# Performance work log

Measured on AMD Instinct MI355X. Metric: run time of the kernel, lower is better.

Reference implementation:

```python
import jax, jax.numpy as jnp
import numpy as np
from jax import lax

# Dimensions (match init_kwargs / input_specs)
S, I, NO = 64, 128, 64      # num_states, num_inputs, num_outputs
K, D = 64, 64               # stack_size, stack_dim
B, T_LEN = 64, 256          # batch of sequences, sequence length
PSTR_THRESH = 0.01          # push/pop gating threshold from original code


def setup_inputs() -> dict:
    key = jax.random.key(0)
    k0, k1, k2, k3, k4, k5 = jax.random.split(key, 6)
    return {
        "input_seq": jax.random.randint(k0, (B, T_LEN), 0, I),
        "T": jax.random.normal(k1, (S, I, D, S), jnp.float32) * 0.1,
        "O": jax.random.normal(k2, (S, I, D, NO), jnp.float32) * 0.1,
        "push_gate": jax.random.normal(k3, (S, I, 1), jnp.float32) * 0.1,
        "pop_gate": jax.random.normal(k4, (S, I, 1), jnp.float32) * 0.1,
        "push_value": jax.random.normal(k5, (S, I, D), jnp.float32) * 0.1,
        "init_logits": jnp.zeros((S,), jnp.float32),
    }


def _run_seq(seq, T, O, push_gate, pop_gate, push_value, init_logits):
    """Process one sequence of int symbols; returns [T_LEN, NO] output probs."""
    state0 = jax.nn.softmax(init_logits)                    # (S,)
    content0 = jnp.zeros((K, D), T.dtype)                   # stack buffer
    pointer0 = jnp.zeros((K,), T.dtype).at[0].set(1.0)      # soft stack pointer

    def step(carry, inp):
        state, content, pointer = carry
        stack_top = pointer @ content                       # (D,) soft read

        # Output: mixture over states of softmax(stack_top @ O[s, inp])
        out_logits = jnp.einsum('d,sdo->so', stack_top, O[:, inp])
        out_prob = state @ jax.nn.softmax(out_logits, axis=-1)  # (NO,)

        # Push/pop strengths: scalars; original uses .item() so they are detached
        push_s = lax.stop_gradient(jax.nn.sigmoid(push_gate[:, inp, 0] @ state))
        pop_s = lax.stop_gradient(jax.nn.sigmoid(pop_gate[:, inp, 0] @ state))
        push_v = jnp.tanh(state @ push_value[:, inp, :])    # (D,) keeps grad

        # Pop (only applied if pop_s > threshold, as in original)
        shifted_down = jnp.concatenate([pointer[1:], jnp.zeros((1,), pointer.dtype)])
        ptr_pop = pop_s * shifted_down + (1.0 - pop_s) * pointer
        pointer = jnp.where(pop_s > PSTR_THRESH, ptr_pop, pointer)

        # Push (only applied if push_s > threshold)
        shifted_up = jnp.concatenate([jnp.zeros((1,), pointer.dtype), pointer[:-1]])
        ptr_push = push_s * shifted_up + (1.0 - push_s) * pointer
        w = ptr_push[:, None]                                # (K,1) write weights
        do_push = push_s > PSTR_THRESH
        pointer = jnp.where(do_push, ptr_push, pointer)
        content = jnp.where(do_push, content * (1.0 - w) + push_v[None, :] * w, content)

        # State transition uses PRE-update stack_top (as in original)
        trans_logits = jnp.einsum('d,sdn->sn', stack_top, T[:, inp])
        new_state = state @ jax.nn.softmax(trans_logits, axis=-1)
        return (new_state, content, pointer), out_prob

    _, outs = lax.scan(step, (state0, content0, pointer0), seq)
    return outs


def reference(input_seq, T, O, push_gate, pop_gate, push_value, init_logits):
    run = lambda seq: _run_seq(seq, T, O, push_gate, pop_gate, push_value, init_logits)
    return jax.vmap(run)(input_seq)  # (B, T_LEN, NO)
```

## Files before the change

kernel.cpp:

```cpp
#include <hip/hip_runtime.h>
#include <math.h>

namespace {
constexpr int cS = 64, cI = 128, cNO = 64, cK = 64, cD = 64, cB = 64, cT = 256;
constexpr float cTH = 0.01f;
constexpr int NTASK = cB * cT;
constexpr int NSPLIT = 8;
typedef float vf4 __attribute__((ext_vector_type(4)));

__device__ inline void st_agent(float* p, float v) {
    __hip_atomic_store(p, v, __ATOMIC_RELAXED, __HIP_MEMORY_SCOPE_AGENT);
}
__device__ inline float ld_agent(const float* p) {
    return __hip_atomic_load(p, __ATOMIC_RELAXED, __HIP_MEMORY_SCOPE_AGENT);
}

__global__ __launch_bounds__(256, 2)
void p1_kernel(const int* __restrict__ seq,
               const float* __restrict__ Tm,
               const float* __restrict__ pgate,
               const float* __restrict__ qgate,
               const float* __restrict__ pval,
               const float* __restrict__ initl,
               float* __restrict__ stbuf,
               int* __restrict__ cnt,
               float* __restrict__ gpart)
{
    const int b  = blockIdx.x >> 3;
    const int jw = blockIdx.x & 7;
    const int tid = threadIdx.x;
    const int wave = tid >> 6, lane = tid & 63;
    const int dq = lane >> 4, o4 = lane & 15;

    __shared__ float s_state[cS], s_stack[cD], s_pushv[cD], s_pvpart[cD];
    __shared__ float s_ptr[cK], s_w[cK];
    __shared__ float s_content[cK][cD];
    __shared__ float s_redA[4][64], s_redB[4][64], s_npart[4][64];
    __shared__ int   s_seq[cT];
    __shared__ float s_push, s_pop;

    if (wave == 0) {
        float v = initl[lane];
        float m = v;
        #pragma unroll
        for (int sh = 1; sh < 64; sh <<= 1) m = fmaxf(m, __shfl_xor(m, sh));
        float e = expf(v - m);
        float s = e;
        #pragma unroll
        for (int sh = 1; sh < 64; sh <<= 1) s += __shfl_xor(s, sh);
        s_state[lane] = e / s;
    } else if (wave == 1) {
        s_ptr[lane] = (lane == 0) ? 1.0f : 0.0f;
    }
    for (int i = tid; i < cK * cD; i += 256) (&s_content[0][0])[i] = 0.f;
    s_seq[tid] = seq[b * cT + tid];
    __syncthreads();

    for (int t = 0; t < cT; ++t) {
        const int inp = s_seq[t];

        {
            float accA = 0.f;
            #pragma unroll
            for (int j = 0; j < 16; ++j) {
                int k = wave * 16 + j;
                accA += s_ptr[k] * s_content[k][lane];
            }
            float accB = 0.f;
            #pragma unroll
            for (int j = 0; j < 2; ++j) {
                int k = jw * 8 + wave * 2 + j;
                accB += s_state[k] * pval[((size_t)k * cI + inp) * cD + lane];
            }
            s_redA[wave][lane] = accA;
            s_redB[wave][lane] = accB;
        }
        __syncthreads();

        float* sb = stbuf + (size_t)(b * cT + t) * 128;
        if (wave == 0) {
            float a = s_redA[0][lane] + s_redA[1][lane] + s_redA[2][lane] + s_redA[3][lane];
            s_stack[lane] = a;
            if (jw == 0) { sb[lane] = a; sb[64 + lane] = s_state[lane]; }
        } else if (wave == 1) {
            s_pvpart[lane] = s_redB[0][lane] + s_redB[1][lane] + s_redB[2][lane] + s_redB[3][lane];
        } else if (wave == 2) {
            float v = pgate[lane * cI + inp] * s_state[lane];
            #pragma unroll
            for (int sh = 1; sh < 64; sh <<= 1) v += __shfl_xor(v, sh);
            if (lane == 0) s_push = 1.0f / (1.0f + expf(-v));
        } else {
            float v = qgate[lane * cI + inp] * s_state[lane];
            #pragma unroll
            for (int sh = 1; sh < 64; sh <<= 1) v += __shfl_xor(v, sh);
            if (lane == 0) s_pop = 1.0f / (1.0f + expf(-v));
        }
        __syncthreads();

        {
            float xs[16];
            #pragma unroll
            for (int i = 0; i < 16; ++i) xs[i] = s_stack[dq * 16 + i];

            const int sA = jw * 8 + wave * 2;
            const int sB = sA + 1;
            const vf4* rpA = reinterpret_cast<const vf4*>(
                Tm + (size_t)(sA * cI + inp) * (cD * cS)) + o4;
            const vf4* rpB = reinterpret_cast<const vf4*>(
                Tm + (size_t)(sB * cI + inp) * (cD * cS)) + o4;
            vf4 va[16], vb[16];
            #pragma unroll
            for (int i = 0; i < 16; ++i) {
                va[i] = rpA[(dq * 16 + i) * 16];
                vb[i] = rpB[(dq * 16 + i) * 16];
            }
            vf4 aA, aB;
            aA.x = 0.f; aA.y = 0.f; aA.z = 0.f; aA.w = 0.f;
            aB.x = 0.f; aB.y = 0.f; aB.z = 0.f; aB.w = 0.f;
            #pragma unroll
            for (int i = 0; i < 16; ++i) {
                float x = xs[i];
                aA.x = fmaf(x, va[i].x, aA.x); aA.y = fmaf(x, va[i].y, aA.y);
                aA.z = fmaf(x, va[i].z, aA.z); aA.w = fmaf(x, va[i].w, aA.w);
                aB.x = fmaf(x, vb[i].x, aB.x); aB.y = fmaf(x, vb[i].y, aB.y);
                aB.z = fmaf(x, vb[i].z, aB.z); aB.w = fmaf(x, vb[i].w, aB.w);
            }
            #pragma unroll
            for (int m = 16; m < 64; m <<= 1) {
                aA.x += __shfl_xor(aA.x, m); aA.y += __shfl_xor(aA.y, m);
                aA.z += __shfl_xor(aA.z, m); aA.w += __shfl_xor(aA.w, m);
                aB.x += __shfl_xor(aB.x, m); aB.y += __shfl_xor(aB.y, m);
                aB.z += __shfl_xor(aB.z, m); aB.w += __shfl_xor(aB.w, m);
            }
            float mA = fmaxf(fmaxf(aA.x, aA.y), fmaxf(aA.z, aA.w));
            float mB = fmaxf(fmaxf(aB.x, aB.y), fmaxf(aB.z, aB.w));
            #pragma unroll
            for (int m = 1; m < 16; m <<= 1) {
                mA = fmaxf(mA, __shfl_xor(mA, m));
                mB = fmaxf(mB, __shfl_xor(mB, m));
            }
            vf4 eA, eB;
            eA.x = expf(aA.x - mA); eA.y = expf(aA.y - mA);
            eA.z = expf(aA.z - mA); eA.w = expf(aA.w - mA);
            eB.x = expf(aB.x - mB); eB.y = expf(aB.y - mB);
            eB.z = expf(aB.z - mB); eB.w = expf(aB.w - mB);
            float smA = eA.x + eA.y + eA.z + eA.w;
            float smB = eB.x + eB.y + eB.z + eB.w;
            #pragma unroll
            for (int m = 1; m < 16; m <<= 1) {
                smA += __shfl_xor(smA, m);
                smB += __shfl_xor(smB, m);
            }
            float cA = s_state[sA] / smA;
            float cB = s_state[sB] / smB;
            vf4 nacc;
            nacc.x = cA * eA.x + cB * eB.x;
            nacc.y = cA * eA.y + cB * eB.y;
            nacc.z = cA * eA.z + cB * eB.z;
            nacc.w = cA * eA.w + cB * eB.w;
            if (dq == 0) {
                s_npart[wave][o4 * 4 + 0] = nacc.x;
                s_npart[wave][o4 * 4 + 1] = nacc.y;
                s_npart[wave][o4 * 4 + 2] = nacc.z;
                s_npart[wave][o4 * 4 + 3] = nacc.w;
            }
        }
        __syncthreads();

        if (wave == 0) {
            float* gq = gpart + ((size_t)(b * 2 + (t & 1)) * NSPLIT + jw) * 128;
            float np = s_npart[0][lane] + s_npart[1][lane] + s_npart[2][lane] + s_npart[3][lane];
            st_agent(gq + lane, np);
            st_agent(gq + 64 + lane, s_pvpart[lane]);
            asm volatile("s_waitcnt vmcnt(0)" ::: "memory");
            int* c = cnt + b * cT + t;
            if (lane == 0)
                __hip_atomic_fetch_add(c, 1, __ATOMIC_RELAXED, __HIP_MEMORY_SCOPE_AGENT);
            while (__hip_atomic_load(c, __ATOMIC_RELAXED, __HIP_MEMORY_SCOPE_AGENT) < NSPLIT) {}
            const float* gb = gpart + (size_t)(b * 2 + (t & 1)) * NSPLIT * 128;
            float ns = 0.f, pvs = 0.f;
            #pragma unroll
            for (int q = 0; q < NSPLIT; ++q) {
                ns  += ld_agent(gb + q * 128 + lane);
                pvs += ld_agent(gb + q * 128 + 64 + lane);
            }
            s_state[lane] = ns;
            s_pushv[lane] = tanhf(pvs);
        } else if (wave == 1) {
            float p  = s_ptr[lane];
            float sd = (lane < cK - 1) ? s_ptr[lane + 1] : 0.f;
            float pop = s_pop;
            float ppo = pop * sd + (1.f - pop) * p;
            float p2  = (pop > cTH) ? ppo : p;
            float su  = __shfl_up(p2, 1);
            if (lane == 0) su = 0.f;
            float push = s_push;
            float ppu = push * su + (1.f - push) * p2;
            s_w[lane] = ppu;
            s_ptr[lane] = (push > cTH) ? ppu : p2;
        }
        __syncthreads();

        if (s_push > cTH) {
            #pragma unroll
            for (int it = 0; it < 16; ++it) {
                int idx = tid + it * 256;
                int k = idx >> 6, d = idx & 63;
                float w = s_w[k];
                s_content[k][d] = s_content[k][d] * (1.f - w) + s_pushv[d] * w;
            }
        }
        __syncthreads();
    }
}

__global__ void k_count(const int* __restrict__ seq, int* __restrict__ counts) {
    int i = blockIdx.x * 256 + threadIdx.x;
    if (i < NTASK) atomicAdd(&counts[seq[i]], 1);
}
__global__ void k_scan(const int* __restrict__ counts, int* __restrict__ offsets,
                       int* __restrict__ cursor) {
    const int lane = threadIdx.x & 63;
    int c0 = counts[lane], c1 = counts[64 + lane];
    int s0 = c0, s1 = c1;
    #pragma unroll
    for (int m = 1; m < 64; m <<= 1) {
        int t0 = __shfl_up(s0, m);
        int t1 = __shfl_up(s1, m);
        if (lane >= m) { s0 += t0; s1 += t1; }
    }
    int tot0 = __shfl(s0, 63);
    int e0 = s0 - c0;
    int e1 = tot0 + s1 - c1;
    offsets[lane] = e0;       cursor[lane] = e0;
    offsets[64 + lane] = e1;  cursor[64 + lane] = e1;
    if (lane == 63) offsets[128] = tot0 + __shfl(s1, 63);
}
__global__ void k_scatter(const int* __restrict__ seq, int* __restrict__ cursor,
                          int* __restrict__ tasks) {
    int i = blockIdx.x * 256 + threadIdx.x;
    if (i < NTASK) {
        int pos = atomicAdd(&cursor[seq[i]], 1);
        tasks[pos] = i;
    }
}

__global__ __launch_bounds__(512, 2)
void p2_kernel(const float* __restrict__ Om,
               const float* __restrict__ stbuf,
               const int* __restrict__ offsets,
               const int* __restrict__ tasks,
               float* __restrict__ out)
{
    const int g = blockIdx.x >> 1, h = blockIdx.x & 1;
    const int tid = threadIdx.x, wave = tid >> 6, lane = tid & 63;
    const int dq = lane >> 4, o4 = lane & 15;

    const int beg = offsets[g], end = offsets[g + 1];
    const int n = end - beg, half = (n + 1) >> 1;
    const int hbeg = beg + h * half;
    const int hend = h ? end : (beg + half);
    const int cnt = hend - hbeg;
    if (cnt <= 0) return;
    const int nsweep = (cnt + 63) >> 6;

    __shared__ vf4 sO[2][1024];

    const vf4* O0 = reinterpret_cast<const vf4*>(Om) + (size_t)g * 1024;
    const size_t rowstride = (size_t)cI * 1024;

    for (int sweep = 0; sweep < nsweep; ++sweep) {
        int   tsk[8];
        bool  val[8];
        float stv[8][16];
        float sstate[8];
        vf4   acc[8];
        #pragma unroll
        for (int u = 0; u < 8; ++u) {
            int idx = hbeg + sweep * 64 + (u >> 2) * 32 + wave * 4 + (u & 3);
            bool v = idx < hend;
            val[u] = v;
            int id = tasks[v ? idx : hbeg];
            id = __builtin_amdgcn_readfirstlane(id);
            tsk[u] = id;
            const float* sp = stbuf + (size_t)id * 128;
            #pragma unroll
            for (int i = 0; i < 16; ++i) stv[u][i] = sp[dq * 16 + i];
            sstate[u] = sp[64 + lane];
            acc[u].x = 0.f; acc[u].y = 0.f; acc[u].z = 0.f; acc[u].w = 0.f;
        }

        vf4 r0 = __builtin_nontemporal_load(O0 + (size_t)tid * 2);
        vf4 r1 = __builtin_nontemporal_load(O0 + (size_t)tid * 2 + 1);

        for (int s = 0; s < cS; ++s) {
            sO[s & 1][tid * 2]     = r0;
            sO[s & 1][tid * 2 + 1] = r1;
            __syncthreads();
            if (s + 1 < cS) {
                const vf4* nr = O0 + (size_t)(s + 1) * rowstride;
                r0 = __builtin_nontemporal_load(nr + (size_t)tid * 2);
                r1 = __builtin_nontemporal_load(nr + (size_t)tid * 2 + 1);
            }
            vf4 part[8];
            #pragma unroll
            for (int u = 0; u < 8; ++u) { part[u].x = 0.f; part[u].y = 0.f; part[u].z = 0.f; part[u].w = 0.f; }
            #pragma unroll
            for (int i = 0; i < 16; ++i) {
                vf4 ovi = sO[s & 1][(dq * 16 + i) * 16 + o4];
                #pragma unroll
                for (int u = 0; u < 8; ++u) {
                    float x = stv[u][i];
                    part[u].x = fmaf(x, ovi.x, part[u].x);
                    part[u].y = fmaf(x, ovi.y, part[u].y);
                    part[u].z = fmaf(x, ovi.z, part[u].z);
                    part[u].w = fmaf(x, ovi.w, part[u].w);
                }
            }
            #pragma unroll
            for (int u = 0; u < 8; ++u) {
                vf4 a = part[u];
                #pragma unroll
                for (int m = 16; m < 64; m <<= 1) {
                    a.x += __shfl_xor(a.x, m); a.y += __shfl_xor(a.y, m);
                    a.z += __shfl_xor(a.z, m); a.w += __shfl_xor(a.w, m);
                }
                float mx = fmaxf(fmaxf(a.x, a.y), fmaxf(a.z, a.w));
                #pragma unroll
                for (int m = 1; m < 16; m <<= 1) mx = fmaxf(mx, __shfl_xor(mx, m));
                vf4 e;
                e.x = expf(a.x - mx); e.y = expf(a.y - mx);
                e.z = expf(a.z - mx); e.w = expf(a.w - mx);
                float sm = e.x + e.y + e.z + e.w;
                #pragma unroll
                for (int m = 1; m < 16; m <<= 1) sm += __shfl_xor(sm, m);
                float coef = __shfl(sstate[u], s) / sm;
                acc[u].x = fmaf(coef, e.x, acc[u].x);
                acc[u].y = fmaf(coef, e.y, acc[u].y);
                acc[u].z = fmaf(coef, e.z, acc[u].z);
                acc[u].w = fmaf(coef, e.w, acc[u].w);
            }
        }
        #pragma unroll
        for (int u = 0; u < 8; ++u) {
            if (val[u] && dq == 0) {
                float* op = out + (size_t)tsk[u] * cNO + o4 * 4;
                op[0] = acc[u].x; op[1] = acc[u].y; op[2] = acc[u].z; op[3] = acc[u].w;
            }
        }
    }
}

__global__ __launch_bounds__(512, 1)
void fpt_mono(const int* __restrict__ seq, const float* __restrict__ Tm,
              const float* __restrict__ Om, const float* __restrict__ pgate,
              const float* __restrict__ qgate, const float* __restrict__ pval,
              const float* __restrict__ initl, float* __restrict__ out)
{
    const int b = blockIdx.x;
    const int tid = threadIdx.x;
    const int wave = tid >> 6, lane = tid & 63;
    const int dq = lane >> 4, o4 = lane & 15;

    __shared__ float s_state[cS], s_nstate[cS], s_stack[cD], s_pushv[cD];
    __shared__ float s_ptr[cK], s_ptr2[cK], s_w[cK];
    __shared__ float s_content[cK][cD];
    __shared__ float s_redA[8][64], s_redB[8][64];
    __shared__ float s_opart[4][cNO], s_npart[4][cS];
    __shared__ float s_push, s_pop;

    if (wave == 0) {
        float v = initl[lane];
        float m = v;
        #pragma unroll
        for (int sh = 1; sh < 64; sh <<= 1) m = fmaxf(m, __shfl_xor(m, sh));
        float e = expf(v - m);
        float s = e;
        #pragma unroll
        for (int sh = 1; sh < 64; sh <<= 1) s += __shfl_xor(s, sh);
        s_state[lane] = e / s;
    } else if (wave == 1) s_ptr[lane] = (lane == 0) ? 1.0f : 0.0f;
    for (int idx = tid; idx < cK * cD; idx += 512) (&s_content[0][0])[idx] = 0.0f;
    __syncthreads();

    for (int t = 0; t < cT; ++t) {
        const int inp = seq[b * cT + t];
        {
            float accA = 0.f, accB = 0.f;
            #pragma unroll
            for (int j = 0; j < 8; ++j) {
                int k = wave * 8 + j;
                accA += s_ptr[k] * s_content[k][lane];
                accB += s_state[k] * pval[(k * cI + inp) * cD + lane];
            }
            s_redA[wave][lane] = accA;
            s_redB[wave][lane] = accB;
        }
        __syncthreads();
        if (wave == 0) {
            float a = 0.f;
            #pragma unroll
            for (int g = 0; g < 8; ++g) a += s_redA[g][lane];
            s_stack[lane] = a;
        } else if (wave == 1) {
            float a = 0.f;
            #pragma unroll
            for (int g = 0; g < 8; ++g) a += s_redB[g][lane];
            s_pushv[lane] = tanhf(a);
        } else if (wave == 2) {
            float v = pgate[lane * cI + inp] * s_state[lane];
            #pragma unroll
            for (int sh = 1; sh < 64; sh <<= 1) v += __shfl_xor(v, sh);
            if (lane == 0) s_push = 1.0f / (1.0f + expf(-v));
        } else if (wave == 3) {
            float v = qgate[lane * cI + inp] * s_state[lane];
            #pragma unroll
            for (int sh = 1; sh < 64; sh <<= 1) v += __shfl_xor(v, sh);
            if (lane == 0) s_pop = 1.0f / (1.0f + expf(-v));
        }
        __syncthreads();
        {
            const bool isO = (wave < 4);
            const int w4 = wave & 3;
            const float* Mbase = isO ? Om : Tm;
            float xs[16];
            #pragma unroll
            for (int i = 0; i < 16; ++i) xs[i] = s_stack[dq * 16 + i];
            float4 oacc = make_float4(0.f, 0.f, 0.f, 0.f);
            for (int r = 0; r < 16; ++r) {
                const int s = w4 * 16 + r;
                const float4* rowp =
                    reinterpret_cast<const float4*>(Mbase + (size_t)(s * cI + inp) * (cD * 64)) + o4;
                float4 acc = make_float4(0.f, 0.f, 0.f, 0.f);
                #pragma unroll
                for (int i = 0; i < 16; ++i) {
                    float4 mv = rowp[(dq * 16 + i) * 16];
                    float xd = xs[i];
                    acc.x = fmaf(xd, mv.x, acc.x); acc.y = fmaf(xd, mv.y, acc.y);
                    acc.z = fmaf(xd, mv.z, acc.z); acc.w = fmaf(xd, mv.w, acc.w);
                }
                #pragma unroll
                for (int m = 16; m < 64; m <<= 1) {
                    acc.x += __shfl_xor(acc.x, m); acc.y += __shfl_xor(acc.y, m);
                    acc.z += __shfl_xor(acc.z, m); acc.w += __shfl_xor(acc.w, m);
                }
                float mx = fmaxf(fmaxf(acc.x, acc.y), fmaxf(acc.z, acc.w));
                #pragma unroll
                for (int m = 1; m < 16; m <<= 1) mx = fmaxf(mx, __shfl_xor(mx, m));
                float4 e;
                e.x = expf(acc.x - mx); e.y = expf(acc.y - mx);
                e.z = expf(acc.z - mx); e.w = expf(acc.w - mx);
                float sm = e.x + e.y + e.z + e.w;
                #pragma unroll
                for (int m = 1; m < 16; m <<= 1) sm += __shfl_xor(sm, m);
                float coef = s_state[s] / sm;
                oacc.x = fmaf(coef, e.x, oacc.x); oacc.y = fmaf(coef, e.y, oacc.y);
                oacc.z = fmaf(coef, e.z, oacc.z); oacc.w = fmaf(coef, e.w, oacc.w);
            }
            if (dq == 0) {
                float* dst = isO ? &s_opart[w4][0] : &s_npart[w4][0];
                dst[o4 * 4 + 0] = oacc.x; dst[o4 * 4 + 1] = oacc.y;
                dst[o4 * 4 + 2] = oacc.z; dst[o4 * 4 + 3] = oacc.w;
            }
        }
        __syncthreads();
        if (wave == 0) {
            float o = s_opart[0][lane] + s_opart[1][lane] + s_opart[2][lane] + s_opart[3][lane];
            out[((size_t)b * cT + t) * cNO + lane] = o;
        } else if (wave == 1) {
            s_nstate[lane] = s_npart[0][lane] + s_npart[1][lane] + s_npart[2][lane] + s_npart[3][lane];
        } else if (wave == 2) {
            float p = s_ptr[lane];
            float sd = (lane < cK - 1) ? s_ptr[lane + 1] : 0.f;
            float pop = s_pop;
            float pp = pop * sd + (1.f - pop) * p;
            s_ptr2[lane] = (pop > cTH) ? pp : p;
        }
        __syncthreads();
        if (wave == 0) {
            float p2 = s_ptr2[lane];
            float su = (lane > 0) ? s_ptr2[lane - 1] : 0.f;
            float push = s_push;
            float pp = push * su + (1.f - push) * p2;
            s_w[lane] = pp;
            s_ptr[lane] = (push > cTH) ? pp : p2;
        } else if (wave == 1) {
            s_state[lane] = s_nstate[lane];
        }
        __syncthreads();
        if (s_push > cTH) {
            for (int idx = tid; idx < cK * cD; idx += 512) {
                int k = idx >> 6, d = idx & 63;
                float w = s_w[k];
                s_content[k][d] = s_content[k][d] * (1.f - w) + s_pushv[d] * w;
            }
        }
        __syncthreads();
    }
}
}

extern "C" void kernel_launch(void* const* d_in, const int* in_sizes, int n_in,
                              void* d_out, int out_size, void* d_ws, size_t ws_size,
                              hipStream_t stream) {
    const int*   seq = (const int*)d_in[0];
    const float* Tm  = (const float*)d_in[1];
    const float* Om  = (const float*)d_in[2];
    const float* pg  = (const float*)d_in[3];
    const float* qg  = (const float*)d_in[4];
    const float* pv  = (const float*)d_in[5];
    const float* il  = (const float*)d_in[6];
    float* o = (float*)d_out;

    const size_t stbuf_bytes  = (size_t)NTASK * 128 * sizeof(float);
    const size_t counts_off   = stbuf_bytes;
    const size_t offsets_off  = counts_off + 128 * sizeof(int);
    const size_t cursor_off   = offsets_off + 132 * sizeof(int);
    const size_t tasks_off    = cursor_off + 128 * sizeof(int);
    const size_t cnt_off      = tasks_off + (size_t)NTASK * sizeof(int);
    const size_t gpart_off    = cnt_off + (size_t)NTASK * sizeof(int);
    const size_t need         = gpart_off + (size_t)cB * 2 * NSPLIT * 128 * sizeof(float);

    if (ws_size < need) {
        hipLaunchKernelGGL(fpt_mono, dim3(cB), dim3(512), 0, stream,
                           seq, Tm, Om, pg, qg, pv, il, o);
        return;
    }

    float* stbuf  = (float*)d_ws;
    int* counts   = (int*)((char*)d_ws + counts_off);
    int* offsets  = (int*)((char*)d_ws + offsets_off);
    int* cursor   = (int*)((char*)d_ws + cursor_off);
    int* tasks    = (int*)((char*)d_ws + tasks_off);
    int* cnt      = (int*)((char*)d_ws + cnt_off);
    float* gpart  = (float*)((char*)d_ws + gpart_off);

    hipMemsetAsync(counts, 0, 128 * sizeof(int), stream);
    hipMemsetAsync(cnt, 0, (size_t)NTASK * sizeof(int), stream);
    hipLaunchKernelGGL(k_count,   dim3(NTASK / 256), dim3(256), 0, stream, seq, counts);
    hipLaunchKernelGGL(k_scan,    dim3(1),           dim3(64),  0, stream, counts, offsets, cursor);
    hipLaunchKernelGGL(k_scatter, dim3(NTASK / 256), dim3(256), 0, stream, seq, cursor, tasks);
    hipLaunchKernelGGL(p1_kernel, dim3(cB * NSPLIT), dim3(256), 0, stream,
                       seq, Tm, pg, qg, pv, il, stbuf, cnt, gpart);
    hipLaunchKernelGGL(p2_kernel, dim3(256), dim3(512), 0, stream, Om, stbuf, offsets, tasks, o);
}
```

Baseline: 2.690 ms.

## Split each sequence's state rows across 16 blocks instead of 8

Each sequence is now handled by 16 cooperating blocks, each computing one transition state row per wave instead of two. Occupancy is raised to 4 blocks per CU to fit twice the block count. This halves per-step global loads and FMAs per block, shortening the serial per-timestep critical path. In exchange, the cross-block reduction and counter-based synchronisation now span more participants, which adds inter-block sync latency and requires all 1024 blocks to be co-resident. The rest of the kernel must also handle 16 partials; that code is not visible here.

```diff
diff --git a/kernel.cpp b/kernel.cpp
--- a/kernel.cpp
+++ b/kernel.cpp
@@ -5,7 +5,7 @@
 constexpr int cS = 64, cI = 128, cNO = 64, cK = 64, cD = 64, cB = 64, cT = 256;
 constexpr float cTH = 0.01f;
 constexpr int NTASK = cB * cT;
-constexpr int NSPLIT = 8;
+constexpr int NSPLIT = 16;
 typedef float vf4 __attribute__((ext_vector_type(4)));
 
 __device__ inline void st_agent(float* p, float v) {
@@ -15,7 +15,7 @@
     return __hip_atomic_load(p, __ATOMIC_RELAXED, __HIP_MEMORY_SCOPE_AGENT);
 }
 
-__global__ __launch_bounds__(256, 2)
+__global__ __launch_bounds__(256, 4)
 void p1_kernel(const int* __restrict__ seq,
                const float* __restrict__ Tm,
                const float* __restrict__ pgate,
@@ -26,11 +26,12 @@
                int* __restrict__ cnt,
                float* __restrict__ gpart)
 {
-    const int b  = blockIdx.x >> 3;
-    const int jw = blockIdx.x & 7;
+    const int b  = blockIdx.x >> 4;
+    const int jw = blockIdx.x & 15;
     const int tid = threadIdx.x;
     const int wave = tid >> 6, lane = tid & 63;
     const int dq = lane >> 4, o4 = lane & 15;
+    const int srow = jw * 4 + wave;
 
     __shared__ float s_state[cS], s_stack[cD], s_pushv[cD], s_pvpart[cD];
     __shared__ float s_ptr[cK], s_w[cK];
@@ -66,12 +67,7 @@
                 int k = wave * 16 + j;
                 accA += s_ptr[k] * s_content[k][lane];
             }
-            float accB = 0.f;
-            #pragma unroll
-            for (int j = 0; j < 2; ++j) {
-                int k = jw * 8 + wave * 2 + j;
-                accB += s_state[k] * pval[((size_t)k * cI + inp) * cD + lane];
-            }
+            float accB = s_state[srow] * pval[((size_t)srow * cI + inp) * cD + lane];
             s_redA[wave][lane] = accA;
             s_redB[wave][lane] = accB;
         }
@@ -102,62 +98,40 @@
             #pragma unroll
             for (int i = 0; i < 16; ++i) xs[i] = s_stack[dq * 16 + i];
 
-            const int sA = jw * 8 + wave * 2;
-            const int sB = sA + 1;
-            const vf4* rpA = reinterpret_cast<const vf4*>(
-                Tm + (size_t)(sA * cI + inp) * (cD * cS)) + o4;
-            const vf4* rpB = reinterpret_cast<const vf4*>(
-                Tm + (size_t)(sB * cI + inp) * (cD * cS)) + o4;
-            vf4 va[16], vb[16];
-            #pragma unroll
-            for (int i = 0; i < 16; ++i) {
-                va[i] = rpA[(dq * 16 + i) * 16];
-                vb[i] = rpB[(dq * 16 + i) * 16];
-            }
-            vf4 aA, aB;
-            aA.x = 0.f; aA.y = 0.f; aA.z = 0.f; aA.w = 0.f;
-            aB.x = 0.f; aB.y = 0.f; aB.z = 0.f; aB.w = 0.f;
+            const vf4* rp = reinterpret_cast<const vf4*>(
+                Tm + (size_t)(srow * cI + inp) * (cD * cS)) + o4;
+            vf4 va[16];
+            #pragma unroll
+            for (int i = 0; i < 16; ++i) va[i] = rp[(dq * 16 + i) * 16];
+
+            vf4 a;
+            a.x = 0.f; a.y = 0.f; a.z = 0.f; a.w = 0.f;
             #pragma unroll
             for (int i = 0; i < 16; ++i) {
                 float x = xs[i];
-                aA.x = fmaf(x, va[i].x, aA.x); aA.y = fmaf(x, va[i].y, aA.y);
-                aA.z = fmaf(x, va[i].z, aA.z); aA.w = fmaf(x, va[i].w, aA.w);
-                aB.x = fmaf(x, vb[i].x, aB.x); aB.y = fmaf(x, vb[i].y, aB.y);
-                aB.z = fmaf(x, vb[i].z, aB.z); aB.w = fmaf(x, vb[i].w, aB.w);
+                a.x = fmaf(x, va[i].x, a.x); a.y = fmaf(x, va[i].y, a.y);
+                a.z = fmaf(x, va[i].z, a.z); a.w = fmaf(x, va[i].w, a.w);
             }
             #pragma unroll
             for (int m = 16; m < 64; m <<= 1) {
-                aA.x += __shfl_xor(aA.x, m); aA.y += __shfl_xor(aA.y, m);
-                aA.z += __shfl_xor(aA.z, m); aA.w += __shfl_xor(aA.w, m);
-                aB.x += __shfl_xor(aB.x, m); aB.y += __shfl_xor(aB.y, m);
-                aB.z += __shfl_xor(aB.z, m); aB.w += __shfl_xor(aB.w, m);
-            }
-            float mA = fmaxf(fmaxf(aA.x, aA.y), fmaxf(aA.z, aA.w));
-            float mB = fmaxf(fmaxf(aB.x, aB.y), fmaxf(aB.z, aB.w));
-            #pragma unroll
-            for (int m = 1; m < 16; m <<= 1) {
-                mA = fmaxf(mA, __shfl_xor(mA, m));
-                mB = fmaxf(mB, __shfl_xor(mB, m));
-            }
-            vf4 eA, eB;
-            eA.x = expf(aA.x - mA); eA.y = expf(aA.y - mA);
-            eA.z = expf(aA.z - mA); eA.w = expf(aA.w - mA);
-            eB.x = expf(aB.x - mB); eB.y = expf(aB.y - mB);
-            eB.z = expf(aB.z - mB); eB.w = expf(aB.w - mB);
-            float smA = eA.x + eA.y + eA.z + eA.w;
-            float smB = eB.x + eB.y + eB.z + eB.w;
-            #pragma unroll
-            for (int m = 1; m < 16; m <<= 1) {
-                smA += __shfl_xor(smA, m);
-                smB += __shfl_xor(smB, m);
-            }
-            float cA = s_state[sA] / smA;
-            float cB = s_state[sB] / smB;
+                a.x += __shfl_xor(a.x, m); a.y += __shfl_xor(a.y, m);
+                a.z += __shfl_xor(a.z, m); a.w += __shfl_xor(a.w, m);
+            }
+            float mx = fmaxf(fmaxf(a.x, a.y), fmaxf(a.z, a.w));
+            #pragma unroll
+            for (int m = 1; m < 16; m <<= 1) mx = fmaxf(mx, __shfl_xor(mx, m));
+            vf4 e;
+            e.x = expf(a.x - mx); e.y = expf(a.y - mx);
+            e.z = expf(a.z - mx); e.w = expf(a.w - mx);
+            float sm = e.x + e.y + e.z + e.w;
+            #pragma unroll
+            for (int m = 1; m < 16; m <<= 1) sm += __shfl_xor(sm, m);
+            float coef = s_state[srow] / sm;
             vf4 nacc;
-            nacc.x = cA * eA.x + cB * eB.x;
-            nacc.y = cA * eA.y + cB * eB.y;
-            nacc.z = cA * eA.z + cB * eB.z;
-            nacc.w = cA * eA.w + cB * eB.w;
+            nacc.x = coef * e.x;
+            nacc.y = coef * e.y;
+            nacc.z = coef * e.z;
+            nacc.w = coef * e.w;
             if (dq == 0) {
                 s_npart[wave][o4 * 4 + 0] = nacc.x;
                 s_npart[wave][o4 * 4 + 1] = nacc.y;
```

Measured after the change: 3.543 ms. +31.7%, slower.

## Defer cross-block state spin-wait and compute push value locally per block

Applied to the files above, without the earlier changes.

Each block now computes the full push_value reduction over all 64 states itself instead of splitting it across the 8 cooperating blocks. That removes the push-vector partials from the global exchange. The spin-wait on the other blocks' new-state partials moves to the start of the next step, where it overlaps with the stack-top read done by the other waves. This shrinks the global handoff and hides the wait, at the cost of 8x more reads of the push_value rows per block.

```diff
diff --git a/kernel.cpp b/kernel.cpp
--- a/kernel.cpp
+++ b/kernel.cpp
@@ -32,7 +32,7 @@
     const int wave = tid >> 6, lane = tid & 63;
     const int dq = lane >> 4, o4 = lane & 15;
 
-    __shared__ float s_state[cS], s_stack[cD], s_pushv[cD], s_pvpart[cD];
+    __shared__ float s_state[cS], s_stack[cD], s_pushv[cD];
     __shared__ float s_ptr[cK], s_w[cK];
     __shared__ float s_content[cK][cD];
     __shared__ float s_redA[4][64], s_redB[4][64], s_npart[4][64];
@@ -59,41 +59,68 @@
     for (int t = 0; t < cT; ++t) {
         const int inp = s_seq[t];
 
+        if (wave == 0) {
+            if (t > 0) {
+                int* c = cnt + b * cT + (t - 1);
+                while (__hip_atomic_load(c, __ATOMIC_RELAXED, __HIP_MEMORY_SCOPE_AGENT) < NSPLIT) {}
+                const float* gb = gpart + (size_t)(b * 2 + ((t - 1) & 1)) * NSPLIT * 64;
+                float ns = 0.f;
+                #pragma unroll
+                for (int q = 0; q < NSPLIT; ++q) ns += ld_agent(gb + q * 64 + lane);
+                s_state[lane] = ns;
+            }
+        } else if (wave == 1) {
+            float a0 = 0.f, a1 = 0.f;
+            #pragma unroll
+            for (int j = 0; j < 16; ++j) a0 += s_ptr[j] * s_content[j][lane];
+            #pragma unroll
+            for (int j = 0; j < 16; ++j) a1 += s_ptr[16 + j] * s_content[16 + j][lane];
+            s_redA[0][lane] = a0;
+            s_redA[1][lane] = a1;
+        } else if (wave == 2) {
+            float a2 = 0.f;
+            #pragma unroll
+            for (int j = 0; j < 16; ++j) a2 += s_ptr[32 + j] * s_content[32 + j][lane];
+            s_redA[2][lane] = a2;
+        } else {
+            float a3 = 0.f;
+            #pragma unroll
+            for (int j = 0; j < 16; ++j) a3 += s_ptr[48 + j] * s_content[48 + j][lane];
+            s_redA[3][lane] = a3;
+        }
+        __syncthreads();
+
         {
-            float accA = 0.f;
+            float accB = 0.f;
             #pragma unroll
             for (int j = 0; j < 16; ++j) {
                 int k = wave * 16 + j;
-                accA += s_ptr[k] * s_content[k][lane];
-            }
-            float accB = 0.f;
-            #pragma unroll
-            for (int j = 0; j < 2; ++j) {
-                int k = jw * 8 + wave * 2 + j;
                 accB += s_state[k] * pval[((size_t)k * cI + inp) * cD + lane];
             }
-            s_redA[wave][lane] = accA;
             s_redB[wave][lane] = accB;
         }
-        __syncthreads();
-
+        if (wave == 2) {
+            float v = pgate[lane * cI + inp] * s_state[lane];
+            #pragma unroll
+            for (int sh = 1; sh < 64; sh <<= 1) v += __shfl_xor(v, sh);
+            if (lane == 0) s_push = 1.0f / (1.0f + expf(-v));
+        } else if (wave == 3) {
+            float v = qgate[lane * cI + inp] * s_state[lane];
+            #pragma unroll
+            for (int sh = 1; sh < 64; sh <<= 1) v += __shfl_xor(v, sh);
+            if (lane == 0) s_pop = 1.0f / (1.0f + expf(-v));
+        }
         float* sb = stbuf + (size_t)(b * cT + t) * 128;
+        if (jw == 0 && wave == 0) sb[64 + lane] = s_state[lane];
+        __syncthreads();
+
         if (wave == 0) {
             float a = s_redA[0][lane] + s_redA[1][lane] + s_redA[2][lane] + s_redA[3][lane];
             s_stack[lane] = a;
-            if (jw == 0) { sb[lane] = a; sb[64 + lane] = s_state[lane]; }
+            if (jw == 0) sb[lane] = a;
         } else if (wave == 1) {
-            s_pvpart[lane] = s_redB[0][lane] + s_redB[1][lane] + s_redB[2][lane] + s_redB[3][lane];
-        } else if (wave == 2) {
-            float v = pgate[lane * cI + inp] * s_state[lane];
-            #pragma unroll
-            for (int sh = 1; sh < 64; sh <<= 1) v += __shfl_xor(v, sh);
-            if (lane == 0) s_push = 1.0f / (1.0f + expf(-v));
-        } else {
-            float v = qgate[lane * cI + inp] * s_state[lane];
-            #pragma unroll
-            for (int sh = 1; sh < 64; sh <<= 1) v += __shfl_xor(v, sh);
-            if (lane == 0) s_pop = 1.0f / (1.0f + expf(-v));
+            s_pushv[lane] = tanhf(s_redB[0][lane] + s_redB[1][lane] +
+                                  s_redB[2][lane] + s_redB[3][lane]);
         }
         __syncthreads();
 
@@ -168,24 +195,12 @@
         __syncthreads();
 
         if (wave == 0) {
-            float* gq = gpart + ((size_t)(b * 2 + (t & 1)) * NSPLIT + jw) * 128;
+            float* gq = gpart + ((size_t)(b * 2 + (t & 1)) * NSPLIT + jw) * 64;
             float np = s_npart[0][lane] + s_npart[1][lane] + s_npart[2][lane] + s_npart[3][lane];
             st_agent(gq + lane, np);
-            st_agent(gq + 64 + lane, s_pvpart[lane]);
             asm volatile("s_waitcnt vmcnt(0)" ::: "memory");
-            int* c = cnt + b * cT + t;
             if (lane == 0)
-                __hip_atomic_fetch_add(c, 1, __ATOMIC_RELAXED, __HIP_MEMORY_SCOPE_AGENT);
-            while (__hip_atomic_load(c, __ATOMIC_RELAXED, __HIP_MEMORY_SCOPE_AGENT) < NSPLIT) {}
-            const float* gb = gpart + (size_t)(b * 2 + (t & 1)) * NSPLIT * 128;
-            float ns = 0.f, pvs = 0.f;
-            #pragma unroll
-            for (int q = 0; q < NSPLIT; ++q) {
-                ns  += ld_agent(gb + q * 128 + lane);
-                pvs += ld_agent(gb + q * 128 + 64 + lane);
-            }
-            s_state[lane] = ns;
-            s_pushv[lane] = tanhf(pvs);
+                __hip_atomic_fetch_add(cnt + b * cT + t, 1, __ATOMIC_RELAXED, __HIP_MEMORY_SCOPE_AGENT);
         } else if (wave == 1) {
             float p  = s_ptr[lane];
             float sd = (lane < cK - 1) ? s_ptr[lane + 1] : 0.f;
@@ -519,7 +534,7 @@
     const size_t tasks_off    = cursor_off + 128 * sizeof(int);
     const size_t cnt_off      = tasks_off + (size_t)NTASK * sizeof(int);
     const size_t gpart_off    = cnt_off + (size_t)NTASK * sizeof(int);
-    const size_t need         = gpart_off + (size_t)cB * 2 * NSPLIT * 128 * sizeof(float);
+    const size_t need         = gpart_off + (size_t)cB * 2 * NSPLIT * 64 * sizeof(float);
 
     if (ws_size < need) {
         hipLaunchKernelGGL(fpt_mono, dim3(cB), dim3(512), 0, stream,
```

Result: slower. 2.800 ms (+4.1%).
